# Optimization experiments

Measured on AMD Instinct MI355X. Metric: run time of the kernel, lower is better.

## Reference

```python
import jax, jax.numpy as jnp
import numpy as np

HEADS = 4
DIM_HEAD = 32
NUM_GROUPS = 8
EPS = 1e-5


def setup_inputs() -> dict:
    key = jax.random.key(0)
    k1, k2, k3, k4 = jax.random.split(key, 4)
    dim = 256
    hidden = HEADS * DIM_HEAD  # 128
    x = jax.random.normal(k1, (4, dim, 64, 64), dtype=jnp.float32)
    # 1x1 convs stored as plain matrices [out_ch, in_ch]
    w_qkv = jax.random.normal(k2, (hidden * 3, dim), dtype=jnp.float32) * (1.0 / np.sqrt(dim))
    w_out = jax.random.normal(k3, (dim, hidden), dtype=jnp.float32) * (1.0 / np.sqrt(hidden))
    b_out = jnp.zeros((dim,), dtype=jnp.float32)
    gamma = jnp.ones((dim,), dtype=jnp.float32)
    beta = jnp.zeros((dim,), dtype=jnp.float32)
    return {"x": x, "w_qkv": w_qkv, "w_out": w_out, "b_out": b_out, "gamma": gamma, "beta": beta}


def group_norm(x, gamma, beta):
    b, c, h, w = x.shape
    xg = x.reshape(b, NUM_GROUPS, c // NUM_GROUPS, h, w)
    mean = xg.mean(axis=(2, 3, 4), keepdims=True)
    var = xg.var(axis=(2, 3, 4), keepdims=True)
    xg = (xg - mean) * jax.lax.rsqrt(var + EPS)
    x = xg.reshape(b, c, h, w)
    return x * gamma[None, :, None, None] + beta[None, :, None, None]


def reference(x, w_qkv, w_out, b_out, gamma, beta):
    b, c, h, w = x.shape
    n = h * w
    scale = DIM_HEAD ** -0.5
    xn = group_norm(x, gamma, beta)  # [b,c,h,w]
    # 1x1 conv QKV: [b, 3*hidden, n]
    qkv = jnp.einsum('oc,bchw->bohw', w_qkv, xn).reshape(b, 3 * HEADS * DIM_HEAD, n)
    q, k, v = jnp.split(qkv, 3, axis=1)
    # -> [b, heads, dim_head, n]
    q = q.reshape(b, HEADS, DIM_HEAD, n) * scale
    k = k.reshape(b, HEADS, DIM_HEAD, n)
    v = v.reshape(b, HEADS, DIM_HEAD, n)
    sim = jnp.einsum('bhdi,bhdj->bhij', q, k)  # [b,heads,n,n]
    sim = sim - jax.lax.stop_gradient(jnp.max(sim, axis=-1, keepdims=True))
    attn = jax.nn.softmax(sim, axis=-1)
    out = jnp.einsum('bhij,bhdj->bhid', attn, v)  # [b,heads,n,dim_head]
    # 'b h (x y) d -> b (h d) x y'
    out = out.transpose(0, 1, 3, 2).reshape(b, HEADS * DIM_HEAD, h, w)
    out = jnp.einsum('oc,bchw->bohw', w_out, out) + b_out[None, :, None, None]
    return out
```

## Files before the change

### kernel.cpp

```cpp
#include <hip/hip_runtime.h>
#include <hip/hip_bf16.h>

typedef float f32x4 __attribute__((ext_vector_type(4)));
typedef short s16x8 __attribute__((ext_vector_type(8)));

__device__ __forceinline__ short f2bf(float f){
  union { float f; unsigned u; } v; v.f = f;
  unsigned u = v.u;
  u += 0x7fffu + ((u >> 16) & 1u);
  return (short)(u >> 16);
}

__device__ __forceinline__ f32x4 mfma16(s16x8 a, s16x8 b, f32x4 c){
  return __builtin_amdgcn_mfma_f32_16x16x32_bf16(a, b, c, 0, 0, 0);
}

__device__ __forceinline__ float fexp2(float x){
#if __has_builtin(__builtin_amdgcn_exp2f)
  return __builtin_amdgcn_exp2f(x);
#else
  float r; asm("v_exp_f32 %0, %1" : "=v"(r) : "v"(x)); return r;
#endif
}

__device__ __forceinline__ unsigned cvtpk(float lo, float hi){
  unsigned r; asm("v_cvt_pk_bf16_f32 %0, %1, %2" : "=v"(r) : "v"(lo), "v"(hi));
  return r;
}

__global__ __launch_bounds__(256) void gn_stats_cvt_k(const float* __restrict__ x,
                                                      const float* __restrict__ wq,
                                                      const float* __restrict__ wo,
                                                      float* __restrict__ part,
                                                      short* __restrict__ wq_bf,
                                                      short* __restrict__ wo_bf){
  int bx = blockIdx.x;
  if (bx >= 1024){
    int i = (bx - 1024)*256 + threadIdx.x;
    if (i < 384*256) wq_bf[i] = f2bf(wq[i]);
    if (i < 256*128) wo_bf[i] = f2bf(wo[i]);
    return;
  }
  const float4* base = ((const float4*)x) + (size_t)bx * 1024;
  float s = 0.f, s2 = 0.f;
  #pragma unroll
  for (int i = threadIdx.x; i < 1024; i += 256){
    float4 v = base[i];
    s  += v.x + v.y + v.z + v.w;
    s2 += v.x*v.x + v.y*v.y + v.z*v.z + v.w*v.w;
  }
  #pragma unroll
  for (int off = 32; off; off >>= 1){ s += __shfl_down(s, off); s2 += __shfl_down(s2, off); }
  __shared__ float ls[8];
  int wid = threadIdx.x >> 6;
  if ((threadIdx.x & 63) == 0){ ls[wid] = s; ls[4 + wid] = s2; }
  __syncthreads();
  if (threadIdx.x == 0){
    part[bx*2]     = ls[0]+ls[1]+ls[2]+ls[3];
    part[bx*2 + 1] = ls[4]+ls[5]+ls[6]+ls[7];
  }
}

__global__ __launch_bounds__(256) void gn_qkv_k(const float* __restrict__ x,
                                                const float* __restrict__ part,
                                                const float* __restrict__ gamma,
                                                const float* __restrict__ beta,
                                                const short* __restrict__ wq_bf,
                                                short* __restrict__ q,
                                                short* __restrict__ k,
                                                short* __restrict__ vt){
  __shared__ float stg[64][33];
  __shared__ short xl[32*264];
  __shared__ float mstat[16];
  int b = blockIdx.y;
  int p0 = blockIdx.x * 32;
  int t = threadIdx.x;
  {
    int gi = t >> 5, sl = t & 31;
    float S  = part[((b*8+gi)*32 + sl)*2];
    float S2 = part[((b*8+gi)*32 + sl)*2 + 1];
    #pragma unroll
    for (int m = 16; m; m >>= 1){ S += __shfl_xor(S, m); S2 += __shfl_xor(S2, m); }
    if (sl == 0){
      float mn = S * (1.f/131072.f);
      mstat[gi]   = mn;
      mstat[8+gi] = rsqrtf(S2 * (1.f/131072.f) - mn*mn + 1e-5f);
    }
  }
  __syncthreads();
  int pj = t & 31, ci8 = t >> 5;
  for (int cc = 0; cc < 4; ++cc){
    #pragma unroll
    for (int r = 0; r < 8; ++r){
      int cl = r*8 + ci8;
      int c = cc*64 + cl;
      float v = x[((size_t)(b*256 + c))*4096 + p0 + pj];
      int gl = c >> 5;
      v = (v - mstat[gl]) * mstat[8+gl] * gamma[c] + beta[c];
      stg[cl][pj] = v;
    }
    __syncthreads();
    {
      s16x8 pack;
      #pragma unroll
      for (int i = 0; i < 8; ++i) pack[i] = f2bf(stg[ci8*8 + i][pj]);
      *(s16x8*)&xl[pj*264 + cc*64 + ci8*8] = pack;
    }
    __syncthreads();
  }
  int w = t >> 6, l = t & 63, l15 = l & 15, g = l >> 4;
  const float QSC = 0.17677669529663687f * 1.4426950408889634f;
  #pragma unroll
  for (int ot = 0; ot < 6; ++ot){
    int orow = w*96 + ot*16 + l15;
    const s16x8* wrow = (const s16x8*)(wq_bf + (size_t)orow * 256);
    s16x8 af[8];
    #pragma unroll
    for (int kk = 0; kk < 8; ++kk) af[kk] = wrow[kk*4 + g];
    #pragma unroll
    for (int pt = 0; pt < 2; ++pt){
      f32x4 acc = {0.f,0.f,0.f,0.f};
      #pragma unroll
      for (int kk = 0; kk < 8; ++kk)
        acc = mfma16(af[kk], *(const s16x8*)&xl[(pt*16+l15)*264 + kk*32 + g*8], acc);
      int p = p0 + pt*16 + l15;
      int pp = p & 31;
      int pos = ((pp>>2)&3)*8 + ((pp>>4)&1)*4 + (pp&3);
      int pperm = (p & ~31) | pos;
      #pragma unroll
      for (int e = 0; e < 4; ++e){
        int og = w*96 + ot*16 + 4*g + e;
        float v = acc[e];
        int sec = og >> 7;
        int oh = og & 127;
        int h = oh >> 5, d = oh & 31;
        size_t qk_idx = (((size_t)b*4 + h)*4096 + p)*32 + d;
        if (sec == 0)      q[qk_idx] = f2bf(v * QSC);
        else if (sec == 1) k[qk_idx] = f2bf(v);
        else vt[(((size_t)b*4 + h)*32 + d)*4096 + pperm] = f2bf(v);
      }
    }
  }
}

__global__ __launch_bounds__(256, 4) void flash_k(const short* __restrict__ q,
                                                  const short* __restrict__ k,
                                                  const short* __restrict__ vt,
                                                  short* __restrict__ at){
  __shared__ short ldsS[4*4096];
  int bid = blockIdx.x;
  int lin = (bid & 7)*128 + (bid >> 3);
  int bh = lin >> 6;
  int rt  = lin & 63;
  int b = bh >> 2, h = bh & 3;
  int blkrow = rt * 64;
  int t = threadIdx.x;
  int w = t >> 6, l = t & 63, l15 = l & 15, g = l >> 4;

  const short* qb = q  + (size_t)bh * 4096 * 32;
  const short* kb = k  + (size_t)bh * 4096 * 32;
  const short* vb = vt + (size_t)bh * 32 * 4096;

  s16x8 qf[4];
  #pragma unroll
  for (int it = 0; it < 4; ++it)
    qf[it] = *(const s16x8*)(qb + (size_t)(blkrow + it*16 + l15)*32 + 8*g);

  const short ONE = (short)0x3F80;
  const s16x8 ones = {ONE,ONE,ONE,ONE,ONE,ONE,ONE,ONE};

  int wbase = w * 4096;
  int rk = wbase + l15*40 + g*8;
  int rv = wbase + 1280 + l15*40 + g*8;
  int row = l >> 1, hi = (l & 1) * 16;
  int wk = wbase + row*40 + hi;
  int wv = wbase + 1280 + row*40 + hi;

  const short* kq = kb + (size_t)w*32768 + l*16;
  const short* vq = vb + (size_t)row*4096 + w*1024 + hi;

  f32x4 o[4][2], osum[4];
  #pragma unroll
  for (int it = 0; it < 4; ++it){
    o[it][0] = (f32x4){0.f,0.f,0.f,0.f};
    o[it][1] = (f32x4){0.f,0.f,0.f,0.f};
    osum[it] = (f32x4){0.f,0.f,0.f,0.f};
  }
  const f32x4 zero = {0.f,0.f,0.f,0.f};

  s16x8 ka0, ka1, va0, va1;

#define FENCE() asm volatile("" ::: "memory")
#define KVLOAD() do{ ka0 = *(const s16x8*)kq; ka1 = *(const s16x8*)(kq + 8); kq += 1024; \
                     va0 = *(const s16x8*)vq; va1 = *(const s16x8*)(vq + 8); vq += 32; }while(0)
#define KVSTORE() do{ *(s16x8*)&ldsS[wk] = ka0; *(s16x8*)&ldsS[wk + 8] = ka1; \
                      *(s16x8*)&ldsS[wv] = va0; *(s16x8*)&ldsS[wv + 8] = va1; }while(0)
#define COMPUTE() do{ \
    s16x8 kf0 = *(const s16x8*)&ldsS[rk]; \
    s16x8 kf1 = *(const s16x8*)&ldsS[rk + 640]; \
    s16x8 vf0 = *(const s16x8*)&ldsS[rv]; \
    s16x8 vf1 = *(const s16x8*)&ldsS[rv + 640]; \
    _Pragma("unroll") \
    for (int it = 0; it < 4; ++it){ \
      f32x4 s0 = mfma16(kf0, qf[it], zero); \
      f32x4 s1 = mfma16(kf1, qf[it], zero); \
      float p0=fexp2(s0[0]), p1=fexp2(s0[1]), p2=fexp2(s0[2]), p3=fexp2(s0[3]); \
      float p4=fexp2(s1[0]), p5=fexp2(s1[1]), p6=fexp2(s1[2]), p7=fexp2(s1[3]); \
      union { s16x8 v; unsigned u[4]; } pf; \
      pf.u[0] = cvtpk(p0,p1); pf.u[1] = cvtpk(p2,p3); \
      pf.u[2] = cvtpk(p4,p5); pf.u[3] = cvtpk(p6,p7); \
      o[it][0] = mfma16(pf.v, vf0, o[it][0]); \
      o[it][1] = mfma16(pf.v, vf1, o[it][1]); \
      osum[it] = mfma16(pf.v, ones, osum[it]); \
    } \
  }while(0)

  KVLOAD();
  KVSTORE();
  FENCE();
  for (int tt = 0; tt < 31; ++tt){
    KVLOAD();
    COMPUTE();
    FENCE();
    KVSTORE();
    FENCE();
  }
  COMPUTE();
#undef KVLOAD
#undef KVSTORE
#undef COMPUTE

  FENCE();
  float* cw = (float*)&ldsS[wbase];
  #pragma unroll
  for (int it = 0; it < 4; ++it){
    #pragma unroll
    for (int e = 0; e < 4; ++e){
      int r = it*16 + 4*g + e;
      cw[r*17 + l15] = o[it][0][e];
      if (l15 == 0) cw[1088 + r] = osum[it][e];
    }
  }
  __syncthreads();
  int rr = t >> 2, a = t & 3;
  size_t rowbase = ((size_t)b*4096 + blkrow + rr)*128 + h*32;
  float den = 0.f, n0 = 0.f, n1 = 0.f, n2 = 0.f, n3 = 0.f;
  #pragma unroll
  for (int w2 = 0; w2 < 4; ++w2){
    const float* cr = (const float*)&ldsS[w2*4096];
    den += cr[1088 + rr];
    n0 += cr[rr*17 + a*4];
    n1 += cr[rr*17 + a*4 + 1];
    n2 += cr[rr*17 + a*4 + 2];
    n3 += cr[rr*17 + a*4 + 3];
  }
  float inv = 1.f / den;
  { uint2 u; u.x = cvtpk(n0*inv, n1*inv); u.y = cvtpk(n2*inv, n3*inv);
    *(uint2*)(at + rowbase + a*4) = u; }
  __syncthreads();
  #pragma unroll
  for (int it = 0; it < 4; ++it){
    #pragma unroll
    for (int e = 0; e < 4; ++e){
      int r = it*16 + 4*g + e;
      cw[r*17 + l15] = o[it][1][e];
    }
  }
  __syncthreads();
  n0 = 0.f; n1 = 0.f; n2 = 0.f; n3 = 0.f;
  #pragma unroll
  for (int w2 = 0; w2 < 4; ++w2){
    const float* cr = (const float*)&ldsS[w2*4096];
    n0 += cr[rr*17 + a*4];
    n1 += cr[rr*17 + a*4 + 1];
    n2 += cr[rr*17 + a*4 + 2];
    n3 += cr[rr*17 + a*4 + 3];
  }
  { uint2 u; u.x = cvtpk(n0*inv, n1*inv); u.y = cvtpk(n2*inv, n3*inv);
    *(uint2*)(at + rowbase + 16 + a*4) = u; }
}

__global__ __launch_bounds__(256) void out_gemm_k(const short* __restrict__ wo_bf,
                                                  const short* __restrict__ at,
                                                  const float* __restrict__ b_out,
                                                  float* __restrict__ out){
  int b = blockIdx.z;
  int obase = blockIdx.y * 64;
  int pbase = blockIdx.x * 64;
  int t = threadIdx.x, w = t >> 6, l = t & 63, l15 = l & 15, g = l >> 4;
  int orow = obase + w*16 + l15;
  const s16x8* wrow = (const s16x8*)(wo_bf + (size_t)orow * 128);
  s16x8 af[4];
  #pragma unroll
  for (int kk = 0; kk < 4; ++kk) af[kk] = wrow[kk*4 + g];
  #pragma unroll
  for (int pt = 0; pt < 4; ++pt){
    int p = pbase + pt*16 + l15;
    const s16x8* xr = (const s16x8*)(at + ((size_t)b*4096 + p) * 128);
    f32x4 acc = {0.f,0.f,0.f,0.f};
    #pragma unroll
    for (int kk = 0; kk < 4; ++kk) acc = mfma16(af[kk], xr[kk*4 + g], acc);
    #pragma unroll
    for (int e = 0; e < 4; ++e){
      int og = obase + w*16 + 4*g + e;
      out[((size_t)b*256 + og)*4096 + p] = acc[e] + b_out[og];
    }
  }
}

extern "C" void kernel_launch(void* const* d_in, const int* in_sizes, int n_in,
                              void* d_out, int out_size, void* d_ws, size_t ws_size,
                              hipStream_t stream){
  const float* x     = (const float*)d_in[0];
  const float* w_qkv = (const float*)d_in[1];
  const float* w_out = (const float*)d_in[2];
  const float* b_out = (const float*)d_in[3];
  const float* gamma = (const float*)d_in[4];
  const float* beta  = (const float*)d_in[5];
  float* out = (float*)d_out;

  char* ws = (char*)d_ws;
  short* wq_bf = (short*)(ws);
  short* wo_bf = (short*)(ws + 196608);
  short* qbuf  = (short*)(ws + 8652800);
  short* kbuf  = (short*)(ws + 12847104);
  short* vtbuf = (short*)(ws + 17041408);
  short* atbuf = (short*)(ws + 21235712);
  float* part  = (float*)(ws + 21235712);

  hipLaunchKernelGGL(gn_stats_cvt_k, dim3(1408),    dim3(256), 0, stream, x, w_qkv, w_out, part, wq_bf, wo_bf);
  hipLaunchKernelGGL(gn_qkv_k,       dim3(128,4),   dim3(256), 0, stream, x, part, gamma, beta, wq_bf, qbuf, kbuf, vtbuf);
  hipLaunchKernelGGL(flash_k,        dim3(1024),    dim3(256), 0, stream, qbuf, kbuf, vtbuf, atbuf);
  hipLaunchKernelGGL(out_gemm_k,     dim3(64,4,4),  dim3(256), 0, stream, wo_bf, atbuf, b_out, out);
}
```

Measured before the change: 88.51 us.

## Split flash attention over key halves and add a combine kernel

Splits the flash attention kernel across two halves of the key/value sequence, doubling the grid to 2048 blocks. Each block writes an unnormalized bf16 numerator and an fp32 denominator, and a new combine kernel sums the two halves and normalizes. The aim is more parallelism and occupancy, with shared memory cut from 32KB to 20KB per block. The cost is an extra launch, extra global traffic, and rounding the partial numerators to bf16 before they are summed.

```diff
diff --git a/kernel.cpp b/kernel.cpp
--- a/kernel.cpp
+++ b/kernel.cpp
@@ -9,6 +9,12 @@
   unsigned u = v.u;
   u += 0x7fffu + ((u >> 16) & 1u);
   return (short)(u >> 16);
+}
+
+__device__ __forceinline__ float bf2f(short s){
+  union { unsigned u; float f; } v;
+  v.u = ((unsigned)(unsigned short)s) << 16;
+  return v.f;
 }
 
 __device__ __forceinline__ f32x4 mfma16(s16x8 a, s16x8 b, f32x4 c){
@@ -146,20 +152,23 @@
 __global__ __launch_bounds__(256, 4) void flash_k(const short* __restrict__ q,
                                                   const short* __restrict__ k,
                                                   const short* __restrict__ vt,
-                                                  short* __restrict__ at){
-  __shared__ short ldsS[4*4096];
+                                                  short* __restrict__ numbf,
+                                                  float* __restrict__ denacc){
+  __shared__ short ldsS[4*2560];
   int bid = blockIdx.x;
-  int lin = (bid & 7)*128 + (bid >> 3);
-  int bh = lin >> 6;
-  int rt  = lin & 63;
+  int lin = (bid & 7)*256 + (bid >> 3);
+  int jh  = lin & 1;
+  int l2  = lin >> 1;
+  int bh = l2 >> 6;
+  int rt  = l2 & 63;
   int b = bh >> 2, h = bh & 3;
   int blkrow = rt * 64;
   int t = threadIdx.x;
   int w = t >> 6, l = t & 63, l15 = l & 15, g = l >> 4;
 
-  const short* qb = q  + (size_t)bh * 4096 * 32;
-  const short* kb = k  + (size_t)bh * 4096 * 32;
-  const short* vb = vt + (size_t)bh * 32 * 4096;
+  const short* qb = q  + (size_t)bh * 131072;
+  const short* kb = k  + (size_t)bh * 131072;
+  const short* vb = vt + (size_t)bh * 131072;
 
   s16x8 qf[4];
   #pragma unroll
@@ -169,15 +178,15 @@
   const short ONE = (short)0x3F80;
   const s16x8 ones = {ONE,ONE,ONE,ONE,ONE,ONE,ONE,ONE};
 
-  int wbase = w * 4096;
+  int wbase = w * 2560;
   int rk = wbase + l15*40 + g*8;
   int rv = wbase + 1280 + l15*40 + g*8;
   int row = l >> 1, hi = (l & 1) * 16;
   int wk = wbase + row*40 + hi;
   int wv = wbase + 1280 + row*40 + hi;
 
-  const short* kq = kb + (size_t)w*32768 + l*16;
-  const short* vq = vb + (size_t)row*4096 + w*1024 + hi;
+  const short* kq = kb + (size_t)(jh*2048 + w*512)*32 + l*16;
+  const short* vq = vb + (size_t)row*4096 + jh*2048 + w*512 + hi;
 
   f32x4 o[4][2], osum[4];
   #pragma unroll
@@ -218,7 +227,7 @@
   KVLOAD();
   KVSTORE();
   FENCE();
-  for (int tt = 0; tt < 31; ++tt){
+  for (int tt = 0; tt < 15; ++tt){
     KVLOAD();
     COMPUTE();
     FENCE();
@@ -243,20 +252,21 @@
   }
   __syncthreads();
   int rr = t >> 2, a = t & 3;
-  size_t rowbase = ((size_t)b*4096 + blkrow + rr)*128 + h*32;
+  size_t rowch = ((size_t)b*4096 + blkrow + rr)*128 + h*32;
+  size_t nbase = (size_t)jh*2097152 + rowch;
   float den = 0.f, n0 = 0.f, n1 = 0.f, n2 = 0.f, n3 = 0.f;
   #pragma unroll
   for (int w2 = 0; w2 < 4; ++w2){
-    const float* cr = (const float*)&ldsS[w2*4096];
+    const float* cr = (const float*)&ldsS[w2*2560];
     den += cr[1088 + rr];
     n0 += cr[rr*17 + a*4];
     n1 += cr[rr*17 + a*4 + 1];
     n2 += cr[rr*17 + a*4 + 2];
     n3 += cr[rr*17 + a*4 + 3];
   }
-  float inv = 1.f / den;
-  { uint2 u; u.x = cvtpk(n0*inv, n1*inv); u.y = cvtpk(n2*inv, n3*inv);
-    *(uint2*)(at + rowbase + a*4) = u; }
+  { uint2 u; u.x = cvtpk(n0, n1); u.y = cvtpk(n2, n3);
+    *(uint2*)(numbf + nbase + a*4) = u; }
+  if (a == 0) denacc[((size_t)jh*16 + bh)*4096 + blkrow + rr] = den;
   __syncthreads();
   #pragma unroll
   for (int it = 0; it < 4; ++it){
@@ -270,14 +280,34 @@
   n0 = 0.f; n1 = 0.f; n2 = 0.f; n3 = 0.f;
   #pragma unroll
   for (int w2 = 0; w2 < 4; ++w2){
-    const float* cr = (const float*)&ldsS[w2*4096];
+    const float* cr = (const float*)&ldsS[w2*2560];
     n0 += cr[rr*17 + a*4];
     n1 += cr[rr*17 + a*4 + 1];
     n2 += cr[rr*17 + a*4 + 2];
     n3 += cr[rr*17 + a*4 + 3];
   }
-  { uint2 u; u.x = cvtpk(n0*inv, n1*inv); u.y = cvtpk(n2*inv, n3*inv);
-    *(uint2*)(at + rowbase + 16 + a*4) = u; }
+  { uint2 u; u.x = cvtpk(n0, n1); u.y = cvtpk(n2, n3);
+    *(uint2*)(numbf + nbase + 16 + a*4) = u; }
+}
+
+__global__ __launch_bounds__(256) void combine_k(short* __restrict__ numbf,
+                                                 const float* __restrict__ denacc){
+  int idx = blockIdx.x*256 + threadIdx.x;
+  int a = idx & 3;
+  int pl = idx >> 2;
+  int bh = pl >> 12, p = pl & 4095;
+  int b = bh >> 2, h = bh & 3;
+  size_t off = (((size_t)b*4096 + p)*128) + h*32 + a*8;
+  s16x8 x0 = *(const s16x8*)(numbf + off);
+  s16x8 x1 = *(const s16x8*)(numbf + 2097152 + off);
+  float inv = 1.f / (denacc[(size_t)bh*4096 + p] + denacc[65536 + (size_t)bh*4096 + p]);
+  float f[8];
+  #pragma unroll
+  for (int j = 0; j < 8; ++j) f[j] = (bf2f(x0[j]) + bf2f(x1[j])) * inv;
+  union { s16x8 v; unsigned u[4]; } ov;
+  ov.u[0] = cvtpk(f[0], f[1]); ov.u[1] = cvtpk(f[2], f[3]);
+  ov.u[2] = cvtpk(f[4], f[5]); ov.u[3] = cvtpk(f[6], f[7]);
+  *(s16x8*)(numbf + off) = ov.v;
 }
 
 __global__ __launch_bounds__(256) void out_gemm_k(const short* __restrict__ wo_bf,
@@ -320,16 +350,18 @@
   float* out = (float*)d_out;
 
   char* ws = (char*)d_ws;
-  short* wq_bf = (short*)(ws);
-  short* wo_bf = (short*)(ws + 196608);
-  short* qbuf  = (short*)(ws + 8652800);
-  short* kbuf  = (short*)(ws + 12847104);
-  short* vtbuf = (short*)(ws + 17041408);
-  short* atbuf = (short*)(ws + 21235712);
-  float* part  = (float*)(ws + 21235712);
+  short* wq_bf  = (short*)(ws);
+  short* wo_bf  = (short*)(ws + 196608);
+  float* denacc = (float*)(ws + 262144);
+  short* numbf  = (short*)(ws + 786432);
+  short* qbuf   = (short*)(ws + 9175040);
+  short* kbuf   = (short*)(ws + 13369344);
+  short* vtbuf  = (short*)(ws + 17563648);
+  float* part   = (float*)(ws + 21757952);
 
   hipLaunchKernelGGL(gn_stats_cvt_k, dim3(1408),    dim3(256), 0, stream, x, w_qkv, w_out, part, wq_bf, wo_bf);
   hipLaunchKernelGGL(gn_qkv_k,       dim3(128,4),   dim3(256), 0, stream, x, part, gamma, beta, wq_bf, qbuf, kbuf, vtbuf);
-  hipLaunchKernelGGL(flash_k,        dim3(1024),    dim3(256), 0, stream, qbuf, kbuf, vtbuf, atbuf);
-  hipLaunchKernelGGL(out_gemm_k,     dim3(64,4,4),  dim3(256), 0, stream, wo_bf, atbuf, b_out, out);
-}
+  hipLaunchKernelGGL(flash_k,        dim3(2048),    dim3(256), 0, stream, qbuf, kbuf, vtbuf, numbf, denacc);
+  hipLaunchKernelGGL(combine_k,      dim3(1024),    dim3(256), 0, stream, numbf, denacc);
+  hipLaunchKernelGGL(out_gemm_k,     dim3(64,4,4),  dim3(256), 0, stream, wo_bf, numbf, b_out, out);
+}
```

Result: slower. 93.04 us (+5.1%).
